# Performance work log

Hardware: AMD Instinct MI355X
Metric: run time of the kernel (lower is better)

## Reference

```python
import jax, jax.numpy as jnp
import numpy as np
from itertools import permutations

# NOTE: the original torch code has `loss_m = loss_r = loss_i = []`, so all three
# names alias ONE list; RI_loss = 2*sum(L) and Mag_loss = sum(L), giving a total
# of 3*sum(per-speaker r+i+mag losses)/num_spks. We reproduce that factor of 3.

def reference(masks, mixture_real, mixture_imag, target_real, target_imag, input_sizes):
    S, B, M, W, F, T, _ = masks.shape
    filt = jax.lax.complex(masks[..., 0], masks[..., 1])          # [S,B,M,W,F,T]
    mix = jax.lax.complex(mixture_real, mixture_imag)             # [S,B,M,F,T]
    ref_ch = 0
    tgt = jax.lax.complex(target_real[:, :, ref_ch], target_imag[:, :, ref_ch])  # [S,B,F,T]

    # filtering(): unfold W time-shifted copies (zero padded) then MAC over (m,w)
    p = (W - 1) // 2
    mix_pad = jnp.pad(mix, ((0, 0), (0, 0), (0, 0), (0, 0), (p, p)))
    win = jnp.stack([mix_pad[..., w:w + T] for w in range(W)], axis=3)  # [S,B,M,W,F,T]
    out = jnp.einsum('sbmwft,sbmwft->sbft', win, filt)            # [S,B,F,T] complex

    # filtering output is permutation-invariant: build pairwise loss matrix once
    d = tgt[None, :] - out[:, None]                               # [S_out, S_tgt, B, F, T]
    lr = jnp.sum(jnp.abs(d.real), axis=(-1, -2))                  # [S,S,B]
    li = jnp.sum(jnp.abs(d.imag), axis=(-1, -2))
    lm = jnp.sum(jnp.abs(jnp.abs(tgt[None, :]) - jnp.abs(out[:, None])), axis=(-1, -2))
    L = lr + li + lm                                              # [S,S,B]

    perms = list(permutations(range(S)))
    pscore = jnp.stack([3.0 * sum(L[s, pm[s]] for s in range(S)) / S for pm in perms])  # [P,B]
    min_perutt = jnp.min(pscore, axis=0)                          # [B]
    num_utts = input_sizes.shape[0]
    return jnp.sum(min_perutt) / num_utts


def setup_inputs() -> dict:
    key = jax.random.key(0)
    ks = jax.random.split(key, 6)
    S, B, M, W, F, T, C = 2, 4, 4, 3, 257, 512, 4
    masks = jax.random.normal(ks[0], (S, B, M, W, F, T, 2), dtype=jnp.float32)
    mixture_real = jax.random.normal(ks[1], (S, B, M, F, T), dtype=jnp.float32)
    mixture_imag = jax.random.normal(ks[2], (S, B, M, F, T), dtype=jnp.float32)
    target_real = jax.random.normal(ks[3], (S, B, C, F, T), dtype=jnp.float32)
    target_imag = jax.random.normal(ks[4], (S, B, C, F, T), dtype=jnp.float32)
    input_sizes = jax.random.randint(ks[5], (B,), 1, 512).astype(jnp.int64)
    return {"masks": masks, "mixture_real": mixture_real, "mixture_imag": mixture_imag,
            "target_real": target_real, "target_imag": target_imag, "input_sizes": input_sizes}
```

## Files before the change

### kernel.cpp

```cpp
#include <hip/hip_runtime.h>

#define S_SPK 2
#define B_BATCH 4
#define M_MIC 4
#define W_TAP 3
#define F_FREQ 257
#define T_TIME 512
#define C_CH 4
#define FT (F_FREQ * T_TIME)

#define NBLK_X 65
#define NBLK_Y 32
#define NSLOT (NBLK_X * NBLK_Y)

typedef float float4u __attribute__((ext_vector_type(4), aligned(4)));
typedef float float2a __attribute__((ext_vector_type(2), aligned(8)));


__global__ __launch_bounds__(256) void pit_main_kernel(
    const float* __restrict__ masks,
    const float* __restrict__ mixr,
    const float* __restrict__ mixi,
    const float* __restrict__ tgtr,
    const float* __restrict__ tgti,
    float* __restrict__ ws)
{
    const int sb   = blockIdx.y >> 2;
    const int tq   = blockIdx.y & 3;
    const int b    = sb & 3;
    const int wave = threadIdx.x >> 6;
    const int lane = threadIdx.x & 63;
    const int f    = blockIdx.x * 4 + wave;

    float L0 = 0.0f, L1 = 0.0f;

    if (f < F_FREQ) {
        const int t0 = tq * 128 + (lane << 1);
        const long rowBase = (long)f * T_TIME;
        const long mixSB   = (long)sb * M_MIC * FT + rowBase;
        const long mskSB   = (long)sb * M_MIC;

        int tc = t0 - 1;
        tc = tc < 0 ? 0 : tc;
        tc = tc > (T_TIME - 4) ? (T_TIME - 4) : tc;

        float4u wr[M_MIC], wi[M_MIC];
        #pragma unroll
        for (int m = 0; m < M_MIC; ++m) {
            wr[m] = *(const float4u*)(mixr + mixSB + (long)m * FT + tc);
            wi[m] = *(const float4u*)(mixi + mixSB + (long)m * FT + tc);
        }

        float4 q[M_MIC * W_TAP];
        #pragma unroll
        for (int m = 0; m < M_MIC; ++m) {
            #pragma unroll
            for (int w = 0; w < W_TAP; ++w) {
                q[m * W_TAP + w] = *(const float4*)(masks +
                    ((((mskSB + m) * W_TAP + w) * F_FREQ + f) * (long)T_TIME + t0) * 2);
            }
        }

        const long tOff = rowBase + t0;
        const float2a t0r = *(const float2a*)(tgtr + ((long)(0 * B_BATCH + b) * C_CH) * FT + tOff);
        const float2a t0i = *(const float2a*)(tgti + ((long)(0 * B_BATCH + b) * C_CH) * FT + tOff);
        const float2a t1r = *(const float2a*)(tgtr + ((long)(1 * B_BATCH + b) * C_CH) * FT + tOff);
        const float2a t1i = *(const float2a*)(tgti + ((long)(1 * B_BATCH + b) * C_CH) * FT + tOff);

        if (t0 == 0) {
            #pragma unroll
            for (int m = 0; m < M_MIC; ++m) {
                wr[m][3] = wr[m][2]; wr[m][2] = wr[m][1]; wr[m][1] = wr[m][0]; wr[m][0] = 0.0f;
                wi[m][3] = wi[m][2]; wi[m][2] = wi[m][1]; wi[m][1] = wi[m][0]; wi[m][0] = 0.0f;
            }
        } else if (t0 == T_TIME - 2) {
            #pragma unroll
            for (int m = 0; m < M_MIC; ++m) {
                wr[m][0] = wr[m][1]; wr[m][1] = wr[m][2]; wr[m][2] = wr[m][3]; wr[m][3] = 0.0f;
                wi[m][0] = wi[m][1]; wi[m][1] = wi[m][2]; wi[m][2] = wi[m][3]; wi[m][3] = 0.0f;
            }
        }

        float or0 = 0.f, oi0 = 0.f, or1 = 0.f, oi1 = 0.f;
        #pragma unroll
        for (int m = 0; m < M_MIC; ++m) {
            #pragma unroll
            for (int w = 0; w < W_TAP; ++w) {
                const float4 qq = q[m * W_TAP + w];
                or0 += wr[m][w]     * qq.x - wi[m][w]     * qq.y;
                oi0 += wr[m][w]     * qq.y + wi[m][w]     * qq.x;
                or1 += wr[m][w + 1] * qq.z - wi[m][w + 1] * qq.w;
                oi1 += wr[m][w + 1] * qq.w + wi[m][w + 1] * qq.z;
            }
        }

        const float ao0 = sqrtf(or0 * or0 + oi0 * oi0);
        const float ao1 = sqrtf(or1 * or1 + oi1 * oi1);
        const float a00 = sqrtf(t0r[0] * t0r[0] + t0i[0] * t0i[0]);
        const float a01 = sqrtf(t0r[1] * t0r[1] + t0i[1] * t0i[1]);
        const float a10 = sqrtf(t1r[0] * t1r[0] + t1i[0] * t1i[0]);
        const float a11 = sqrtf(t1r[1] * t1r[1] + t1i[1] * t1i[1]);

        L0 = fabsf(t0r[0] - or0) + fabsf(t0i[0] - oi0) + fabsf(a00 - ao0)
           + fabsf(t0r[1] - or1) + fabsf(t0i[1] - oi1) + fabsf(a01 - ao1);
        L1 = fabsf(t1r[0] - or0) + fabsf(t1i[0] - oi0) + fabsf(a10 - ao0)
           + fabsf(t1r[1] - or1) + fabsf(t1i[1] - oi1) + fabsf(a11 - ao1);
    }

    #pragma unroll
    for (int off = 32; off > 0; off >>= 1) {
        L0 += __shfl_down(L0, off, 64);
        L1 += __shfl_down(L1, off, 64);
    }
    __shared__ float s0[4], s1[4];
    if (lane == 0) { s0[wave] = L0; s1[wave] = L1; }
    __syncthreads();
    if (threadIdx.x == 0) {
        const int slot = blockIdx.y * NBLK_X + blockIdx.x;
        ws[slot * 2 + 0] = s0[0] + s0[1] + s0[2] + s0[3];
        ws[slot * 2 + 1] = s1[0] + s1[1] + s1[2] + s1[3];
    }
}

__global__ __launch_bounds__(256) void pit_final_kernel(
    const float* __restrict__ ws, float* __restrict__ out, int num_utts)
{
    float acc[16];
    #pragma unroll
    for (int i = 0; i < 16; ++i) acc[i] = 0.0f;

    for (int slot = threadIdx.x; slot < NSLOT; slot += 256) {
        const int y  = slot / NBLK_X;
        const int sb = y >> 2;
        const int so = sb >> 2;
        const int b  = sb & 3;
        acc[((so * 2 + 0) << 2) + b] += ws[slot * 2 + 0];
        acc[((so * 2 + 1) << 2) + b] += ws[slot * 2 + 1];
    }

    __shared__ float red[16][4];
    const int wave = threadIdx.x >> 6;
    const int lane = threadIdx.x & 63;
    #pragma unroll
    for (int i = 0; i < 16; ++i) {
        float v = acc[i];
        #pragma unroll
        for (int off = 32; off > 0; off >>= 1) v += __shfl_down(v, off, 64);
        if (lane == 0) red[i][wave] = v;
    }
    __syncthreads();

    if (threadIdx.x == 0) {
        float L[16];
        #pragma unroll
        for (int i = 0; i < 16; ++i) L[i] = red[i][0] + red[i][1] + red[i][2] + red[i][3];
        float accu = 0.0f;
        for (int b = 0; b < B_BATCH; ++b) {
            const float pid = L[(0 * 2 + 0) * 4 + b] + L[(1 * 2 + 1) * 4 + b];
            const float psw = L[(0 * 2 + 1) * 4 + b] + L[(1 * 2 + 0) * 4 + b];
            const float sc0 = 3.0f * pid / (float)S_SPK;
            const float sc1 = 3.0f * psw / (float)S_SPK;
            accu += fminf(sc0, sc1);
        }
        out[0] = accu / (float)num_utts;
    }
}

extern "C" void kernel_launch(void* const* d_in, const int* in_sizes, int n_in,
                              void* d_out, int out_size, void* d_ws, size_t ws_size,
                              hipStream_t stream) {
    const float* masks = (const float*)d_in[0];
    const float* mixr  = (const float*)d_in[1];
    const float* mixi  = (const float*)d_in[2];
    const float* tgtr  = (const float*)d_in[3];
    const float* tgti  = (const float*)d_in[4];
    const int num_utts = in_sizes[5];

    float* ws  = (float*)d_ws;
    float* out = (float*)d_out;

    dim3 grid(NBLK_X, NBLK_Y);
    pit_main_kernel<<<grid, 256, 0, stream>>>(masks, mixr, mixi, tgtr, tgti, ws);

    pit_final_kernel<<<1, 256, 0, stream>>>(ws, out, num_utts);
}
```

Baseline: 201.4 us.

## Split filter MAC across waves per (m,w) tap and reduce through shared memory

Each block now handles one (speaker, batch, freq) row of all 512 time steps with 768 threads, where each of 12 waves owns one (mic, tap) pair. Each wave loads its mask row and shifted mixture samples, writes complex products to a 48KB LDS buffer, and after a barrier 512 threads sum the 12 partials and compute the loss. The aim is more parallel memory requests per block and fewer registers per thread. The cost is 48KB of LDS per block, which limits occupancy, plus an extra barrier and an LDS round trip.

```diff
diff --git a/kernel.cpp b/kernel.cpp
--- a/kernel.cpp
+++ b/kernel.cpp
@@ -9,15 +9,13 @@
 #define C_CH 4
 #define FT (F_FREQ * T_TIME)
 
-#define NBLK_X 65
-#define NBLK_Y 32
-#define NSLOT (NBLK_X * NBLK_Y)
+#define NBLK (S_SPK * B_BATCH * F_FREQ)
+#define NSLOT NBLK
 
-typedef float float4u __attribute__((ext_vector_type(4), aligned(4)));
-typedef float float2a __attribute__((ext_vector_type(2), aligned(8)));
+typedef float float2u __attribute__((ext_vector_type(2), aligned(4)));
 
 
-__global__ __launch_bounds__(256) void pit_main_kernel(
+__global__ __launch_bounds__(768) void pit_main_kernel(
     const float* __restrict__ masks,
     const float* __restrict__ mixr,
     const float* __restrict__ mixi,
@@ -25,86 +23,75 @@
     const float* __restrict__ tgti,
     float* __restrict__ ws)
 {
-    const int sb   = blockIdx.y >> 2;
-    const int tq   = blockIdx.y & 3;
+    const int blk  = blockIdx.x;
+    const int sb   = blk / F_FREQ;
+    const int f    = blk - sb * F_FREQ;
     const int b    = sb & 3;
-    const int wave = threadIdx.x >> 6;
+    const int wv   = threadIdx.x >> 6;
     const int lane = threadIdx.x & 63;
-    const int f    = blockIdx.x * 4 + wave;
+    const int m    = wv / 3;
+    const int w    = wv - m * 3;
+
+    __shared__ float part[12][1024];
+
+    const float* mrow = masks + ((long)(sb * 12 + wv) * F_FREQ + f) * (T_TIME * 2);
+    float4 q[4];
+    #pragma unroll
+    for (int c = 0; c < 4; ++c)
+        q[c] = *(const float4*)(mrow + c * 256 + (lane << 2));
+
+    const float* mxr = mixr + ((long)(sb * M_MIC + m) * FT) + (long)f * T_TIME;
+    const float* mxi = mixi + ((long)(sb * M_MIC + m) * FT) + (long)f * T_TIME;
+    float2u xr[4], xi[4];
+    #pragma unroll
+    for (int c = 0; c < 4; ++c) {
+        const int t0 = c * 128 + (lane << 1);
+        int a = t0 + w - 1;
+        a = a < 0 ? 0 : (a > 510 ? 510 : a);
+        xr[c] = *(const float2u*)(mxr + a);
+        xi[c] = *(const float2u*)(mxi + a);
+    }
+    if (w == 0 && lane == 0) {
+        xr[0].y = xr[0].x; xr[0].x = 0.0f;
+        xi[0].y = xi[0].x; xi[0].x = 0.0f;
+    }
+    if (w == 2 && lane == 63) {
+        xr[3].x = xr[3].y; xr[3].y = 0.0f;
+        xi[3].x = xi[3].y; xi[3].y = 0.0f;
+    }
+
+    #pragma unroll
+    for (int c = 0; c < 4; ++c) {
+        float4 o;
+        o.x = xr[c].x * q[c].x - xi[c].x * q[c].y;
+        o.y = xr[c].x * q[c].y + xi[c].x * q[c].x;
+        o.z = xr[c].y * q[c].z - xi[c].y * q[c].w;
+        o.w = xr[c].y * q[c].w + xi[c].y * q[c].z;
+        *(float4*)&part[wv][c * 256 + (lane << 2)] = o;
+    }
+    __syncthreads();
 
     float L0 = 0.0f, L1 = 0.0f;
+    if (threadIdx.x < 512) {
+        const int t = threadIdx.x;
+        float orr = 0.0f, oii = 0.0f;
+        #pragma unroll
+        for (int mw = 0; mw < 12; ++mw) {
+            const float2u p = *(const float2u*)&part[mw][t * 2];
+            orr += p.x;
+            oii += p.y;
+        }
+        const long to = (long)f * T_TIME + t;
+        const float t0r = tgtr[(long)(0 * B_BATCH + b) * C_CH * FT + to];
+        const float t0i = tgti[(long)(0 * B_BATCH + b) * C_CH * FT + to];
+        const float t1r = tgtr[(long)(1 * B_BATCH + b) * C_CH * FT + to];
+        const float t1i = tgti[(long)(1 * B_BATCH + b) * C_CH * FT + to];
 
-    if (f < F_FREQ) {
-        const int t0 = tq * 128 + (lane << 1);
-        const long rowBase = (long)f * T_TIME;
-        const long mixSB   = (long)sb * M_MIC * FT + rowBase;
-        const long mskSB   = (long)sb * M_MIC;
-
-        int tc = t0 - 1;
-        tc = tc < 0 ? 0 : tc;
-        tc = tc > (T_TIME - 4) ? (T_TIME - 4) : tc;
-
-        float4u wr[M_MIC], wi[M_MIC];
-        #pragma unroll
-        for (int m = 0; m < M_MIC; ++m) {
-            wr[m] = *(const float4u*)(mixr + mixSB + (long)m * FT + tc);
-            wi[m] = *(const float4u*)(mixi + mixSB + (long)m * FT + tc);
-        }
-
-        float4 q[M_MIC * W_TAP];
-        #pragma unroll
-        for (int m = 0; m < M_MIC; ++m) {
-            #pragma unroll
-            for (int w = 0; w < W_TAP; ++w) {
-                q[m * W_TAP + w] = *(const float4*)(masks +
-                    ((((mskSB + m) * W_TAP + w) * F_FREQ + f) * (long)T_TIME + t0) * 2);
-            }
-        }
-
-        const long tOff = rowBase + t0;
-        const float2a t0r = *(const float2a*)(tgtr + ((long)(0 * B_BATCH + b) * C_CH) * FT + tOff);
-        const float2a t0i = *(const float2a*)(tgti + ((long)(0 * B_BATCH + b) * C_CH) * FT + tOff);
-        const float2a t1r = *(const float2a*)(tgtr + ((long)(1 * B_BATCH + b) * C_CH) * FT + tOff);
-        const float2a t1i = *(const float2a*)(tgti + ((long)(1 * B_BATCH + b) * C_CH) * FT + tOff);
-
-        if (t0 == 0) {
-            #pragma unroll
-            for (int m = 0; m < M_MIC; ++m) {
-                wr[m][3] = wr[m][2]; wr[m][2] = wr[m][1]; wr[m][1] = wr[m][0]; wr[m][0] = 0.0f;
-                wi[m][3] = wi[m][2]; wi[m][2] = wi[m][1]; wi[m][1] = wi[m][0]; wi[m][0] = 0.0f;
-            }
-        } else if (t0 == T_TIME - 2) {
-            #pragma unroll
-            for (int m = 0; m < M_MIC; ++m) {
-                wr[m][0] = wr[m][1]; wr[m][1] = wr[m][2]; wr[m][2] = wr[m][3]; wr[m][3] = 0.0f;
-                wi[m][0] = wi[m][1]; wi[m][1] = wi[m][2]; wi[m][2] = wi[m][3]; wi[m][3] = 0.0f;
-            }
-        }
-
-        float or0 = 0.f, oi0 = 0.f, or1 = 0.f, oi1 = 0.f;
-        #pragma unroll
-        for (int m = 0; m < M_MIC; ++m) {
-            #pragma unroll
-            for (int w = 0; w < W_TAP; ++w) {
-                const float4 qq = q[m * W_TAP + w];
-                or0 += wr[m][w]     * qq.x - wi[m][w]     * qq.y;
-                oi0 += wr[m][w]     * qq.y + wi[m][w]     * qq.x;
-                or1 += wr[m][w + 1] * qq.z - wi[m][w + 1] * qq.w;
-                oi1 += wr[m][w + 1] * qq.w + wi[m][w + 1] * qq.z;
-            }
-        }
-
-        const float ao0 = sqrtf(or0 * or0 + oi0 * oi0);
-        const float ao1 = sqrtf(or1 * or1 + oi1 * oi1);
-        const float a00 = sqrtf(t0r[0] * t0r[0] + t0i[0] * t0i[0]);
-        const float a01 = sqrtf(t0r[1] * t0r[1] + t0i[1] * t0i[1]);
-        const float a10 = sqrtf(t1r[0] * t1r[0] + t1i[0] * t1i[0]);
-        const float a11 = sqrtf(t1r[1] * t1r[1] + t1i[1] * t1i[1]);
-
-        L0 = fabsf(t0r[0] - or0) + fabsf(t0i[0] - oi0) + fabsf(a00 - ao0)
-           + fabsf(t0r[1] - or1) + fabsf(t0i[1] - oi1) + fabsf(a01 - ao1);
-        L1 = fabsf(t1r[0] - or0) + fabsf(t1i[0] - oi0) + fabsf(a10 - ao0)
-           + fabsf(t1r[1] - or1) + fabsf(t1i[1] - oi1) + fabsf(a11 - ao1);
+        const float ao = sqrtf(orr * orr + oii * oii);
+        const float a0 = sqrtf(t0r * t0r + t0i * t0i);
+        const float a1 = sqrtf(t1r * t1r + t1i * t1i);
+        L0 = fabsf(t0r - orr) + fabsf(t0i - oii) + fabsf(a0 - ao);
+        L1 = fabsf(t1r - orr) + fabsf(t1i - oii) + fabsf(a1 - ao);
     }
 
     #pragma unroll
@@ -112,13 +99,15 @@
         L0 += __shfl_down(L0, off, 64);
         L1 += __shfl_down(L1, off, 64);
     }
-    __shared__ float s0[4], s1[4];
-    if (lane == 0) { s0[wave] = L0; s1[wave] = L1; }
+    __shared__ float s0[12], s1[12];
+    if (lane == 0) { s0[wv] = L0; s1[wv] = L1; }
     __syncthreads();
     if (threadIdx.x == 0) {
-        const int slot = blockIdx.y * NBLK_X + blockIdx.x;
-        ws[slot * 2 + 0] = s0[0] + s0[1] + s0[2] + s0[3];
-        ws[slot * 2 + 1] = s1[0] + s1[1] + s1[2] + s1[3];
+        float a = 0.0f, c = 0.0f;
+        #pragma unroll
+        for (int i = 0; i < 12; ++i) { a += s0[i]; c += s1[i]; }
+        ws[blk * 2 + 0] = a;
+        ws[blk * 2 + 1] = c;
     }
 }
 
@@ -130,8 +119,7 @@
     for (int i = 0; i < 16; ++i) acc[i] = 0.0f;
 
     for (int slot = threadIdx.x; slot < NSLOT; slot += 256) {
-        const int y  = slot / NBLK_X;
-        const int sb = y >> 2;
+        const int sb = slot / F_FREQ;
         const int so = sb >> 2;
         const int b  = sb & 3;
         acc[((so * 2 + 0) << 2) + b] += ws[slot * 2 + 0];
@@ -179,8 +167,7 @@
     float* ws  = (float*)d_ws;
     float* out = (float*)d_out;
 
-    dim3 grid(NBLK_X, NBLK_Y);
-    pit_main_kernel<<<grid, 256, 0, stream>>>(masks, mixr, mixi, tgtr, tgti, ws);
+    pit_main_kernel<<<NBLK, 768, 0, stream>>>(masks, mixr, mixi, tgtr, tgti, ws);
 
     pit_final_kernel<<<1, 256, 0, stream>>>(ws, out, num_utts);
 }
```

Result: faster. 196.1 us (-2.7%).
